# Optimization experiments

Hardware: AMD Instinct MI355X
Metric: run time of the kernel (lower is better)

Reference implementation:

```python
import jax, jax.numpy as jnp
import numpy as np

N_ATOMS = 50000
N_PAIRS = 1600000
F = 128   # per-atom features
NF = 128  # filters
RBF = 20

LOG2 = float(np.log(2.0))

def shifted_softplus(x):
    # SchNet activation: ln(0.5*e^x + 0.5) = softplus(x) - ln(2)
    return jax.nn.softplus(x) - LOG2

def setup_inputs() -> dict:
    key = jax.random.key(0)
    ks = jax.random.split(key, 12)
    inv = lambda n: 1.0 / np.sqrt(n)
    return {
        "atomic_embedding": jax.random.normal(ks[0], (N_ATOMS, F), jnp.float32),
        "pair_indices": jax.random.randint(ks[1], (2, N_PAIRS), 0, N_ATOMS, jnp.int32),
        "f_ij": jax.random.uniform(ks[2], (N_PAIRS, RBF), jnp.float32),
        "f_ij_cutoff": jax.random.uniform(ks[3], (N_PAIRS, 1), jnp.float32),
        # intput_to_feature: Linear(F -> NF, no bias)
        "W_in": jax.random.normal(ks[4], (F, NF), jnp.float32) * inv(F),
        # filter_network: Linear(RBF->NF)+act, Linear(NF->NF)
        "W_f1": jax.random.normal(ks[5], (RBF, NF), jnp.float32) * inv(RBF),
        "b_f1": jnp.zeros((NF,), jnp.float32),
        "W_f2": jax.random.normal(ks[6], (NF, NF), jnp.float32) * inv(NF),
        "b_f2": jnp.zeros((NF,), jnp.float32),
        # feature_to_output: Linear(NF->F)+act, Linear(F->F)
        "W_o1": jax.random.normal(ks[7], (NF, F), jnp.float32) * inv(NF),
        "b_o1": jnp.zeros((F,), jnp.float32),
        "W_o2": jax.random.normal(ks[8], (F, F), jnp.float32) * inv(F),
        "b_o2": jnp.zeros((F,), jnp.float32),
    }

def reference(atomic_embedding, pair_indices, f_ij, f_ij_cutoff,
              W_in, W_f1, b_f1, W_f2, b_f2, W_o1, b_o1, W_o2, b_o2):
    idx_i = pair_indices[0]
    idx_j = pair_indices[1]
    # input projection: [N_ATOMS, NF]
    x = atomic_embedding @ W_in
    # filter network on radial basis: [N_PAIRS, NF]
    W_ij = shifted_softplus(f_ij @ W_f1 + b_f1) @ W_f2 + b_f2
    W_ij = W_ij * f_ij_cutoff  # cutoff-weighted filters
    # gather neighbor features, filter multiply, scatter-add into atoms
    x_ij = x[idx_j] * W_ij  # [N_PAIRS, NF]
    out = jax.ops.segment_sum(x_ij, idx_i, num_segments=N_ATOMS)  # [N_ATOMS, NF]
    # output MLP
    return shifted_softplus(out @ W_o1 + b_o1) @ W_o2 + b_o2
```

## Files before the change

### kernel.cpp

```cpp
#include <hip/hip_runtime.h>

#define NA 50000
#define NP 1600000
#define NT_PAIR (NP / 128)
#define PAIR_BLOCKS 1024

#define WS_X     0
#define WS_W1T   25600000
#define WS_W2T   25610240
#define WS_WINT  25645056
#define WS_WO1T  25679872
#define WS_WO2T  25714688

typedef __attribute__((ext_vector_type(4))) float f32x4;
typedef __attribute__((ext_vector_type(8))) short short8;

#define MFMA(a, b, c) __builtin_amdgcn_mfma_f32_16x16x32_bf16((a), (b), (c), 0, 0, 0)

__device__ __forceinline__ unsigned short f2bf(float f) {
    unsigned int u = __float_as_uint(f);
    u += 0x7FFFu + ((u >> 16) & 1u);
    return (unsigned short)(u >> 16);
}

__device__ __forceinline__ float bf2f(unsigned short h) {
    return __uint_as_float(((unsigned int)h) << 16);
}

__device__ __forceinline__ float ssp_f(float z) {
    float az = fabsf(z);
    float e  = __expf(-az);
    float l  = __logf(1.0f + e);
    return fmaxf(z, 0.0f) + l - 0.69314718056f;
}

template <int LDA, int LDB, int KS, bool SPLIT>
__device__ __forceinline__ void gemm_t(const unsigned short* A, const unsigned short* Al,
                                       const unsigned short* B, int m0, int nc0,
                                       int lr, int lg, f32x4 (&acc)[2][4]) {
#pragma unroll
    for (int ks = 0; ks < KS; ++ks) {
        const int ko = ks * 32 + lg * 8;
        short8 a0 = *(const short8*)(A + (m0 + lr) * LDA + ko);
        short8 a1 = *(const short8*)(A + (m0 + 16 + lr) * LDA + ko);
        short8 a0l, a1l;
        if constexpr (SPLIT) {
            a0l = *(const short8*)(Al + (m0 + lr) * LDA + ko);
            a1l = *(const short8*)(Al + (m0 + 16 + lr) * LDA + ko);
        }
#pragma unroll
        for (int nt = 0; nt < 4; ++nt) {
            short8 b = *(const short8*)(B + (nc0 + nt * 16 + lr) * LDB + ko);
            acc[0][nt] = MFMA(a0, b, acc[0][nt]);
            acc[1][nt] = MFMA(a1, b, acc[1][nt]);
            if constexpr (SPLIT) {
                acc[0][nt] = MFMA(a0l, b, acc[0][nt]);
                acc[1][nt] = MFMA(a1l, b, acc[1][nt]);
            }
        }
    }
}

__global__ void prep_kernel(const float* __restrict__ Wf1, const float* __restrict__ Wf2,
                            const float* __restrict__ Win, const float* __restrict__ Wo1,
                            const float* __restrict__ Wo2, unsigned short* __restrict__ w1t,
                            unsigned short* __restrict__ w2t, unsigned short* __restrict__ wint,
                            unsigned short* __restrict__ wo1t, unsigned short* __restrict__ wo2t) {
    const int n = blockIdx.x;
    const int k = threadIdx.x;
    const int m = blockIdx.y;
    if (m == 0) {
        if (k < 40) w1t[n * 40 + k] = (k < 20) ? f2bf(Wf1[k * 128 + n]) : (unsigned short)0;
    } else {
        const float* src = (m == 1) ? Wf2 : (m == 2) ? Win : (m == 3) ? Wo1 : Wo2;
        unsigned short* dst = (m == 1) ? w2t : (m == 2) ? wint : (m == 3) ? wo1t : wo2t;
        if (k < 136) dst[n * 136 + k] = (k < 128) ? f2bf(src[k * 128 + n]) : (unsigned short)0;
    }
}

__global__ __launch_bounds__(512, 2) void xproj_kernel(const float* __restrict__ emb,
                                                       const unsigned short* __restrict__ wint,
                                                       float* __restrict__ x) {
    __shared__ __align__(16) unsigned short sAh[128 * 136];
    __shared__ __align__(16) unsigned short sAl[128 * 136];
    __shared__ __align__(16) unsigned short sW[128 * 136];
    const int tid = threadIdx.x;
    const int r0 = blockIdx.x * 128;
#pragma unroll
    for (int it = 0; it < 32; ++it) {
        int idx = it * 512 + tid;
        int row = idx >> 7, col = idx & 127;
        int r = r0 + row;
        float v = (r < NA) ? emb[(size_t)r * 128 + col] : 0.0f;
        unsigned short hi = f2bf(v);
        unsigned short lo = f2bf(v - bf2f(hi));
        sAh[row * 136 + col] = hi;
        sAl[row * 136 + col] = lo;
    }
    {
        const unsigned int* s = (const unsigned int*)wint;
        unsigned int* d = (unsigned int*)sW;
        for (int i = tid; i < 128 * 136 / 2; i += 512) d[i] = s[i];
    }
    __syncthreads();
    const int lane = tid & 63, wave = tid >> 6;
    const int lr = lane & 15, lg = lane >> 4;
    const int m0 = (wave & 3) * 32, nc0 = (wave >> 2) * 64;
    f32x4 acc[2][4] = {};
    gemm_t<136, 136, 4, true>(sAh, sAl, sW, m0, nc0, lr, lg, acc);
#pragma unroll
    for (int mt = 0; mt < 2; ++mt)
#pragma unroll
        for (int i = 0; i < 4; ++i) {
            int rl = m0 + mt * 16 + lg * 4 + i;
            int r = r0 + rl;
            if (r < NA) {
#pragma unroll
                for (int nt = 0; nt < 4; ++nt) {
                    int col = nc0 + nt * 16 + lr;
                    x[(size_t)r * 128 + col] = acc[mt][nt][i];
                }
            }
        }
}

__global__ __launch_bounds__(512, 2) void pair_kernel(
        const float* __restrict__ fij, const float* __restrict__ fcut,
        const int* __restrict__ idxI, const int* __restrict__ idxJ,
        const float* __restrict__ x, const unsigned short* __restrict__ w1t,
        const unsigned short* __restrict__ w2t, const float* __restrict__ bf1,
        const float* __restrict__ bf2, float* __restrict__ out) {
    __shared__ __align__(16) unsigned short sW1[128 * 40];
    __shared__ __align__(16) unsigned short sW2[128 * 136];
    __shared__ __align__(16) unsigned short sF[2][128 * 40];
    __shared__ __align__(16) unsigned short sH[128 * 136];
    __shared__ float sB1[128], sB2[128];
    __shared__ float sCut[2][128];
    __shared__ int sII[2][128], sJJ[2][128];

    const int tid = threadIdx.x;
    {
        const unsigned int* s1 = (const unsigned int*)w1t;
        unsigned int* d1 = (unsigned int*)sW1;
        for (int i = tid; i < 128 * 40 / 2; i += 512) d1[i] = s1[i];
        const unsigned int* s2 = (const unsigned int*)w2t;
        unsigned int* d2 = (unsigned int*)sW2;
        for (int i = tid; i < 128 * 136 / 2; i += 512) d2[i] = s2[i];
        if (tid < 128) { sB1[tid] = bf1[tid]; sB2[tid] = bf2[tid]; }
        unsigned int* z = (unsigned int*)&sF[0][0];
        for (int i = tid; i < 2 * 128 * 40 / 2; i += 512) z[i] = 0;
    }
    const int lane = tid & 63, wave = tid >> 6;
    const int lr = lane & 15, lg = lane >> 4;
    const int m0 = (wave & 3) * 32, nc0 = (wave >> 2) * 64;

    int t = blockIdx.x;
    float pf[5];
    int pi = 0, pj = 0;
    float pc = 0.0f;
    auto pref = [&](int T) {
        const float* fp = fij + (size_t)T * 2560;
#pragma unroll
        for (int r = 0; r < 5; ++r) pf[r] = fp[r * 512 + tid];
        if (tid < 128) {
            pi = idxI[T * 128 + tid];
            pj = idxJ[T * 128 + tid];
            pc = fcut[T * 128 + tid];
        }
    };
    pref(t);
    int buf = 0;
    __syncthreads();

    for (; t < NT_PAIR;) {
#pragma unroll
        for (int r = 0; r < 5; ++r) {
            int idx = r * 512 + tid;
            int p = (int)(__umulhi((unsigned)idx, 0xCCCCCCCDu) >> 4);
            int k = idx - p * 20;
            sF[buf][p * 40 + k] = f2bf(pf[r]);
        }
        if (tid < 128) { sII[buf][tid] = pi; sJJ[buf][tid] = pj; sCut[buf][tid] = pc; }
        int tn = t + PAIR_BLOCKS;
        if (tn < NT_PAIR) pref(tn);
        __syncthreads();

        f32x4 acc1[2][4] = {};
        gemm_t<40, 40, 1, false>(&sF[buf][0], nullptr, sW1, m0, nc0, lr, lg, acc1);

#pragma unroll
        for (int mt = 0; mt < 2; ++mt)
#pragma unroll
            for (int nt = 0; nt < 4; ++nt) {
                int col = nc0 + nt * 16 + lr;
                float b1 = sB1[col];
#pragma unroll
                for (int i = 0; i < 4; ++i) {
                    int rl = m0 + mt * 16 + lg * 4 + i;
                    sH[rl * 136 + col] = f2bf(ssp_f(acc1[mt][nt][i] + b1));
                }
            }
        __syncthreads();

        f32x4 acc2[2][4] = {};
        gemm_t<136, 136, 4, false>(sH, nullptr, sW2, m0, nc0, lr, lg, acc2);

#pragma unroll
        for (int mt = 0; mt < 2; ++mt) {
#pragma unroll
            for (int i = 0; i < 4; ++i) {
                int rl = m0 + mt * 16 + lg * 4 + i;
                int ii = sII[buf][rl];
                int jj = sJJ[buf][rl];
                float cc = sCut[buf][rl];
                const float* xr = x + (size_t)jj * 128;
                float* orow = out + (size_t)ii * 128;
#pragma unroll
                for (int nt = 0; nt < 4; ++nt) {
                    int col = nc0 + nt * 16 + lr;
                    float v = (acc2[mt][nt][i] + sB2[col]) * cc * xr[col];
                    unsafeAtomicAdd(&orow[col], v);
                }
            }
        }
        buf ^= 1;
        t = tn;
    }
}

__global__ __launch_bounds__(512, 2) void mlp_kernel(const unsigned short* __restrict__ wo1t,
                                                     const unsigned short* __restrict__ wo2t,
                                                     const float* __restrict__ bo1,
                                                     const float* __restrict__ bo2,
                                                     float* __restrict__ out) {
    __shared__ __align__(16) unsigned short sAh[128 * 136];
    __shared__ __align__(16) unsigned short sAl[128 * 136];
    __shared__ __align__(16) unsigned short sW[128 * 136];
    __shared__ float sb1[128], sb2[128];
    const int tid = threadIdx.x;
    const int r0 = blockIdx.x * 128;
#pragma unroll
    for (int it = 0; it < 32; ++it) {
        int idx = it * 512 + tid;
        int row = idx >> 7, col = idx & 127;
        int r = r0 + row;
        float v = (r < NA) ? out[(size_t)r * 128 + col] : 0.0f;
        unsigned short hi = f2bf(v);
        unsigned short lo = f2bf(v - bf2f(hi));
        sAh[row * 136 + col] = hi;
        sAl[row * 136 + col] = lo;
    }
    {
        const unsigned int* s = (const unsigned int*)wo1t;
        unsigned int* d = (unsigned int*)sW;
        for (int i = tid; i < 128 * 136 / 2; i += 512) d[i] = s[i];
    }
    if (tid < 128) { sb1[tid] = bo1[tid]; sb2[tid] = bo2[tid]; }
    __syncthreads();
    const int lane = tid & 63, wave = tid >> 6;
    const int lr = lane & 15, lg = lane >> 4;
    const int m0 = (wave & 3) * 32, nc0 = (wave >> 2) * 64;

    f32x4 acc[2][4] = {};
    gemm_t<136, 136, 4, true>(sAh, sAl, sW, m0, nc0, lr, lg, acc);
    __syncthreads();

#pragma unroll
    for (int mt = 0; mt < 2; ++mt)
#pragma unroll
        for (int nt = 0; nt < 4; ++nt) {
            int col = nc0 + nt * 16 + lr;
            float b1 = sb1[col];
#pragma unroll
            for (int i = 0; i < 4; ++i) {
                int rl = m0 + mt * 16 + lg * 4 + i;
                sAh[rl * 136 + col] = f2bf(ssp_f(acc[mt][nt][i] + b1));
            }
        }
    {
        const unsigned int* s = (const unsigned int*)wo2t;
        unsigned int* d = (unsigned int*)sW;
        for (int i = tid; i < 128 * 136 / 2; i += 512) d[i] = s[i];
    }
    __syncthreads();

    f32x4 acc2[2][4] = {};
    gemm_t<136, 136, 4, false>(sAh, nullptr, sW, m0, nc0, lr, lg, acc2);
#pragma unroll
    for (int mt = 0; mt < 2; ++mt)
#pragma unroll
        for (int i = 0; i < 4; ++i) {
            int rl = m0 + mt * 16 + lg * 4 + i;
            int r = r0 + rl;
            if (r < NA) {
#pragma unroll
                for (int nt = 0; nt < 4; ++nt) {
                    int col = nc0 + nt * 16 + lr;
                    out[(size_t)r * 128 + col] = acc2[mt][nt][i] + sb2[col];
                }
            }
        }
}

extern "C" void kernel_launch(void* const* d_in, const int* in_sizes, int n_in,
                              void* d_out, int out_size, void* d_ws, size_t ws_size,
                              hipStream_t stream) {
    const float* emb  = (const float*)d_in[0];
    const int*   pidx = (const int*)d_in[1];
    const float* fij  = (const float*)d_in[2];
    const float* fcut = (const float*)d_in[3];
    const float* Win  = (const float*)d_in[4];
    const float* Wf1  = (const float*)d_in[5];
    const float* bf1  = (const float*)d_in[6];
    const float* Wf2  = (const float*)d_in[7];
    const float* bf2  = (const float*)d_in[8];
    const float* Wo1  = (const float*)d_in[9];
    const float* bo1  = (const float*)d_in[10];
    const float* Wo2  = (const float*)d_in[11];
    const float* bo2  = (const float*)d_in[12];
    float* out = (float*)d_out;
    char* ws = (char*)d_ws;

    float* x = (float*)(ws + WS_X);
    unsigned short* w1t  = (unsigned short*)(ws + WS_W1T);
    unsigned short* w2t  = (unsigned short*)(ws + WS_W2T);
    unsigned short* wint = (unsigned short*)(ws + WS_WINT);
    unsigned short* wo1t = (unsigned short*)(ws + WS_WO1T);
    unsigned short* wo2t = (unsigned short*)(ws + WS_WO2T);

    hipMemsetAsync(d_out, 0, (size_t)NA * 128 * sizeof(float), stream);
    prep_kernel<<<dim3(128, 5), 256, 0, stream>>>(Wf1, Wf2, Win, Wo1, Wo2,
                                                  w1t, w2t, wint, wo1t, wo2t);
    xproj_kernel<<<(NA + 127) / 128, 512, 0, stream>>>(emb, wint, x);
    pair_kernel<<<PAIR_BLOCKS, 512, 0, stream>>>(fij, fcut, pidx, pidx + NP, x,
                                                 w1t, w2t, bf1, bf2, out);
    mlp_kernel<<<(NA + 127) / 128, 512, 0, stream>>>(wo1t, wo2t, bo1, bo2, out);
}
```

Before: 1.091 ms.

## Sort pairs by destination atom and accumulate per-atom segments in LDS

New measurement: 1.816 ms. +66.4%, slower.

```diff
diff --git a/kernel.cpp b/kernel.cpp
--- a/kernel.cpp
+++ b/kernel.cpp
@@ -2,15 +2,23 @@
 
 #define NA 50000
 #define NP 1600000
-#define NT_PAIR (NP / 128)
-#define PAIR_BLOCKS 1024
-
-#define WS_X     0
-#define WS_W1T   25600000
-#define WS_W2T   25610240
-#define WS_WINT  25645056
-#define WS_WO1T  25679872
-#define WS_WO2T  25714688
+#define RA 16
+#define NR (NA / RA)
+#define PAIR_BLOCKS 512
+#define NB_SCAN 98
+
+#define WS_X      0
+#define WS_W1T    25600000
+#define WS_W2T    25610240
+#define WS_WINT   25645056
+#define WS_WO1T   25679872
+#define WS_WO2T   25714688
+#define WS_CNT    25749504
+#define WS_START  25949504
+#define WS_CURSOR 26149512
+#define WS_BSUM   26349512
+#define WS_BOFF   26350016
+#define WS_PERM   26350400
 
 typedef __attribute__((ext_vector_type(4))) float f32x4;
 typedef __attribute__((ext_vector_type(8))) short short8;
@@ -22,11 +30,9 @@
     u += 0x7FFFu + ((u >> 16) & 1u);
     return (unsigned short)(u >> 16);
 }
-
 __device__ __forceinline__ float bf2f(unsigned short h) {
     return __uint_as_float(((unsigned int)h) << 16);
 }
-
 __device__ __forceinline__ float ssp_f(float z) {
     float az = fabsf(z);
     float e  = __expf(-az);
@@ -58,6 +64,74 @@
                 acc[1][nt] = MFMA(a1l, b, acc[1][nt]);
             }
         }
+    }
+}
+
+__global__ void hist_kernel(const int* __restrict__ idxI, int* __restrict__ cnt) {
+    int p = blockIdx.x * 512 + threadIdx.x;
+    if (p < NP) atomicAdd(&cnt[idxI[p]], 1);
+}
+
+__global__ void scanA_kernel(const int* __restrict__ cnt, int* __restrict__ bsum) {
+    __shared__ int s[512];
+    int tid = threadIdx.x;
+    int i = blockIdx.x * 512 + tid;
+    s[tid] = (i < NA) ? cnt[i] : 0;
+    __syncthreads();
+#pragma unroll
+    for (int off = 256; off > 0; off >>= 1) {
+        if (tid < off) s[tid] += s[tid + off];
+        __syncthreads();
+    }
+    if (tid == 0) bsum[blockIdx.x] = s[0];
+}
+
+__global__ void scanB_kernel(const int* __restrict__ bsum, int* __restrict__ boff,
+                             int* __restrict__ start) {
+    __shared__ int s[128];
+    int tid = threadIdx.x;
+    int v = (tid < NB_SCAN) ? bsum[tid] : 0;
+    s[tid] = v;
+    __syncthreads();
+#pragma unroll
+    for (int off = 1; off < 128; off <<= 1) {
+        int t = (tid >= off) ? s[tid - off] : 0;
+        __syncthreads();
+        s[tid] += t;
+        __syncthreads();
+    }
+    if (tid < NB_SCAN) boff[tid] = s[tid] - v;
+    if (tid == 0) start[NA] = s[127];
+}
+
+__global__ void scanC_kernel(const int* __restrict__ cnt, const int* __restrict__ boff,
+                             int* __restrict__ start, int* __restrict__ cursor) {
+    __shared__ int s[512];
+    int tid = threadIdx.x;
+    int i = blockIdx.x * 512 + tid;
+    int v = (i < NA) ? cnt[i] : 0;
+    s[tid] = v;
+    __syncthreads();
+#pragma unroll
+    for (int off = 1; off < 512; off <<= 1) {
+        int t = (tid >= off) ? s[tid - off] : 0;
+        __syncthreads();
+        s[tid] += t;
+        __syncthreads();
+    }
+    if (i < NA) {
+        int excl = s[tid] - v + boff[blockIdx.x];
+        start[i] = excl;
+        cursor[i] = excl;
+    }
+}
+
+__global__ void scatter_kernel(const int* __restrict__ idxI, int* __restrict__ cursor,
+                               int* __restrict__ perm) {
+    int p = blockIdx.x * 512 + threadIdx.x;
+    if (p < NP) {
+        int pos = atomicAdd(&cursor[idxI[p]], 1);
+        __hip_atomic_store(&perm[pos], p, __ATOMIC_RELAXED, __HIP_MEMORY_SCOPE_AGENT);
     }
 }
 
@@ -124,107 +198,121 @@
         }
 }
 
-__global__ __launch_bounds__(512, 2) void pair_kernel(
+__global__ __launch_bounds__(256, 2) void pair_kernel(
         const float* __restrict__ fij, const float* __restrict__ fcut,
         const int* __restrict__ idxI, const int* __restrict__ idxJ,
+        const int* __restrict__ start, const int* __restrict__ perm,
         const float* __restrict__ x, const unsigned short* __restrict__ w1t,
         const unsigned short* __restrict__ w2t, const float* __restrict__ bf1,
         const float* __restrict__ bf2, float* __restrict__ out) {
     __shared__ __align__(16) unsigned short sW1[128 * 40];
     __shared__ __align__(16) unsigned short sW2[128 * 136];
-    __shared__ __align__(16) unsigned short sF[2][128 * 40];
-    __shared__ __align__(16) unsigned short sH[128 * 136];
+    __shared__ __align__(16) unsigned short sF[64 * 40];
+    __shared__ __align__(16) unsigned short sH[64 * 136];
+    __shared__ float sAcc[RA * 128];
     __shared__ float sB1[128], sB2[128];
-    __shared__ float sCut[2][128];
-    __shared__ int sII[2][128], sJJ[2][128];
+    __shared__ float sCut[64];
+    __shared__ int sJJ[64], sLa[64];
 
     const int tid = threadIdx.x;
     {
         const unsigned int* s1 = (const unsigned int*)w1t;
         unsigned int* d1 = (unsigned int*)sW1;
-        for (int i = tid; i < 128 * 40 / 2; i += 512) d1[i] = s1[i];
+        for (int i = tid; i < 128 * 40 / 2; i += 256) d1[i] = s1[i];
         const unsigned int* s2 = (const unsigned int*)w2t;
         unsigned int* d2 = (unsigned int*)sW2;
-        for (int i = tid; i < 128 * 136 / 2; i += 512) d2[i] = s2[i];
+        for (int i = tid; i < 128 * 136 / 2; i += 256) d2[i] = s2[i];
         if (tid < 128) { sB1[tid] = bf1[tid]; sB2[tid] = bf2[tid]; }
-        unsigned int* z = (unsigned int*)&sF[0][0];
-        for (int i = tid; i < 2 * 128 * 40 / 2; i += 512) z[i] = 0;
+        unsigned int* z = (unsigned int*)sF;
+        for (int i = tid; i < 64 * 40 / 2; i += 256) z[i] = 0;
     }
     const int lane = tid & 63, wave = tid >> 6;
     const int lr = lane & 15, lg = lane >> 4;
-    const int m0 = (wave & 3) * 32, nc0 = (wave >> 2) * 64;
-
-    int t = blockIdx.x;
-    float pf[5];
-    int pi = 0, pj = 0;
-    float pc = 0.0f;
-    auto pref = [&](int T) {
-        const float* fp = fij + (size_t)T * 2560;
-#pragma unroll
-        for (int r = 0; r < 5; ++r) pf[r] = fp[r * 512 + tid];
-        if (tid < 128) {
-            pi = idxI[T * 128 + tid];
-            pj = idxJ[T * 128 + tid];
-            pc = fcut[T * 128 + tid];
-        }
-    };
-    pref(t);
-    int buf = 0;
-    __syncthreads();
-
-    for (; t < NT_PAIR;) {
-#pragma unroll
-        for (int r = 0; r < 5; ++r) {
-            int idx = r * 512 + tid;
-            int p = (int)(__umulhi((unsigned)idx, 0xCCCCCCCDu) >> 4);
-            int k = idx - p * 20;
-            sF[buf][p * 40 + k] = f2bf(pf[r]);
-        }
-        if (tid < 128) { sII[buf][tid] = pi; sJJ[buf][tid] = pj; sCut[buf][tid] = pc; }
-        int tn = t + PAIR_BLOCKS;
-        if (tn < NT_PAIR) pref(tn);
-        __syncthreads();
-
-        f32x4 acc1[2][4] = {};
-        gemm_t<40, 40, 1, false>(&sF[buf][0], nullptr, sW1, m0, nc0, lr, lg, acc1);
-
-#pragma unroll
-        for (int mt = 0; mt < 2; ++mt)
-#pragma unroll
-            for (int nt = 0; nt < 4; ++nt) {
-                int col = nc0 + nt * 16 + lr;
-                float b1 = sB1[col];
+    const int m0 = (wave & 1) * 32, nc0 = (wave >> 1) * 64;
+    const int srow = tid >> 2, sq = tid & 3;
+
+    for (int r = blockIdx.x; r < NR; r += gridDim.x) {
+        const int a0 = r * RA;
+        const int s = start[a0], e = start[a0 + RA];
+        for (int i = tid; i < RA * 128; i += 256) sAcc[i] = 0.0f;
+        __syncthreads();
+
+        const int ntile = (e - s + 63) >> 6;
+        for (int tl = 0; tl < ntile; ++tl) {
+            const int base = s + tl * 64;
+            {
+                int slot = base + srow;
+                if (slot < e) {
+                    int pid = perm[slot];
+                    const float* fr = fij + (size_t)pid * 20 + sq * 5;
+#pragma unroll
+                    for (int u = 0; u < 5; ++u) sF[srow * 40 + sq * 5 + u] = f2bf(fr[u]);
+                }
+                if (tid < 64) {
+                    int slot2 = base + tid;
+                    if (slot2 < e) {
+                        int pid2 = perm[slot2];
+                        sJJ[tid] = idxJ[pid2];
+                        sCut[tid] = fcut[pid2];
+                        sLa[tid] = idxI[pid2] - a0;
+                    } else { sJJ[tid] = 0; sCut[tid] = 0.0f; sLa[tid] = 0; }
+                }
+            }
+            __syncthreads();
+
+            float xp[2][4][4];
+#pragma unroll
+            for (int mt = 0; mt < 2; ++mt)
 #pragma unroll
                 for (int i = 0; i < 4; ++i) {
                     int rl = m0 + mt * 16 + lg * 4 + i;
-                    sH[rl * 136 + col] = f2bf(ssp_f(acc1[mt][nt][i] + b1));
-                }
-            }
-        __syncthreads();
-
-        f32x4 acc2[2][4] = {};
-        gemm_t<136, 136, 4, false>(sH, nullptr, sW2, m0, nc0, lr, lg, acc2);
-
-#pragma unroll
-        for (int mt = 0; mt < 2; ++mt) {
-#pragma unroll
-            for (int i = 0; i < 4; ++i) {
-                int rl = m0 + mt * 16 + lg * 4 + i;
-                int ii = sII[buf][rl];
-                int jj = sJJ[buf][rl];
-                float cc = sCut[buf][rl];
-                const float* xr = x + (size_t)jj * 128;
-                float* orow = out + (size_t)ii * 128;
+                    const float* xr = x + (size_t)sJJ[rl] * 128;
+#pragma unroll
+                    for (int nt = 0; nt < 4; ++nt)
+                        xp[mt][i][nt] = xr[nc0 + nt * 16 + lr];
+                }
+
+            f32x4 acc1[2][4] = {};
+            gemm_t<40, 40, 1, false>(sF, nullptr, sW1, m0, nc0, lr, lg, acc1);
+
+#pragma unroll
+            for (int mt = 0; mt < 2; ++mt)
 #pragma unroll
                 for (int nt = 0; nt < 4; ++nt) {
                     int col = nc0 + nt * 16 + lr;
-                    float v = (acc2[mt][nt][i] + sB2[col]) * cc * xr[col];
-                    unsafeAtomicAdd(&orow[col], v);
-                }
-            }
-        }
-        buf ^= 1;
-        t = tn;
+                    float b1 = sB1[col];
+#pragma unroll
+                    for (int i = 0; i < 4; ++i) {
+                        int rl = m0 + mt * 16 + lg * 4 + i;
+                        sH[rl * 136 + col] = f2bf(ssp_f(acc1[mt][nt][i] + b1));
+                    }
+                }
+            __syncthreads();
+
+            f32x4 acc2[2][4] = {};
+            gemm_t<136, 136, 4, false>(sH, nullptr, sW2, m0, nc0, lr, lg, acc2);
+
+#pragma unroll
+            for (int mt = 0; mt < 2; ++mt)
+#pragma unroll
+                for (int i = 0; i < 4; ++i) {
+                    int rl = m0 + mt * 16 + lg * 4 + i;
+                    float cc = sCut[rl];
+                    float* arow = &sAcc[sLa[rl] * 128];
+#pragma unroll
+                    for (int nt = 0; nt < 4; ++nt) {
+                        int col = nc0 + nt * 16 + lr;
+                        float v = (acc2[mt][nt][i] + sB2[col]) * cc * xp[mt][i][nt];
+                        atomicAdd(&arow[col], v);
+                    }
+                }
+            __syncthreads();
+        }
+
+        for (int i = tid; i < RA * 128; i += 256) {
+            int la = i >> 7, c = i & 127;
+            out[((size_t)(a0 + la)) * 128 + c] = sAcc[i];
+        }
     }
 }
 
@@ -321,18 +409,33 @@
     float* out = (float*)d_out;
     char* ws = (char*)d_ws;
 
+    const int* idxI = pidx;
+    const int* idxJ = pidx + NP;
+
     float* x = (float*)(ws + WS_X);
     unsigned short* w1t  = (unsigned short*)(ws + WS_W1T);
     unsigned short* w2t  = (unsigned short*)(ws + WS_W2T);
     unsigned short* wint = (unsigned short*)(ws + WS_WINT);
     unsigned short* wo1t = (unsigned short*)(ws + WS_WO1T);
     unsigned short* wo2t = (unsigned short*)(ws + WS_WO2T);
-
-    hipMemsetAsync(d_out, 0, (size_t)NA * 128 * sizeof(float), stream);
+    int* cnt    = (int*)(ws + WS_CNT);
+    int* start  = (int*)(ws + WS_START);
+    int* cursor = (int*)(ws + WS_CURSOR);
+    int* bsum   = (int*)(ws + WS_BSUM);
+    int* boff   = (int*)(ws + WS_BOFF);
+    int* perm   = (int*)(ws + WS_PERM);
+
+    hipMemsetAsync(cnt, 0, NA * sizeof(int), stream);
+    hist_kernel<<<NP / 512, 512, 0, stream>>>(idxI, cnt);
+    scanA_kernel<<<NB_SCAN, 512, 0, stream>>>(cnt, bsum);
+    scanB_kernel<<<1, 128, 0, stream>>>(bsum, boff, start);
+    scanC_kernel<<<NB_SCAN, 512, 0, stream>>>(cnt, boff, start, cursor);
+    scatter_kernel<<<NP / 512, 512, 0, stream>>>(idxI, cursor, perm);
+
     prep_kernel<<<dim3(128, 5), 256, 0, stream>>>(Wf1, Wf2, Win, Wo1, Wo2,
                                                   w1t, w2t, wint, wo1t, wo2t);
     xproj_kernel<<<(NA + 127) / 128, 512, 0, stream>>>(emb, wint, x);
-    pair_kernel<<<PAIR_BLOCKS, 512, 0, stream>>>(fij, fcut, pidx, pidx + NP, x,
+    pair_kernel<<<PAIR_BLOCKS, 256, 0, stream>>>(fij, fcut, idxI, idxJ, start, perm, x,
                                                  w1t, w2t, bf1, bf2, out);
     mlp_kernel<<<(NA + 127) / 128, 512, 0, stream>>>(wo1t, wo2t, bo1, bo2, out);
 }
```
